# Kernel optimization log

Measured on AMD Instinct MI355X. Metric: run time of the kernel, lower is better.

The kernel has to match this reference:

```python
import jax, jax.numpy as jnp
import numpy as np

# dims
B, T, D, H, DFF, NTYPE = 8, 1024, 512, 8, 1024, 341
HD = D // H                    # 64 head dim
NUM_AXES = 1
DPR = D // H // (NUM_AXES + 1) # 32 dims rotated per axis
EPS = 1e-5
THETA = 10000.0


def layernorm(x, g, b):
    m = jnp.mean(x, axis=-1, keepdims=True)
    v = jnp.mean((x - m) ** 2, axis=-1, keepdims=True)
    return (x - m) * jax.lax.rsqrt(v + EPS) * g + b


def swiglu(x):
    a, gate = jnp.split(x, 2, axis=-1)
    return jax.nn.silu(gate) * a


def apply_rope(x, pos):
    # x: [B,H,T,DPR], pos: [B,T] float positions (possibly non-integer / scrambled order)
    inv_freq = 1.0 / (THETA ** (jnp.arange(0, DPR, 2, dtype=jnp.float32) / DPR))  # [DPR/2]
    freqs = pos[:, None, :, None] * inv_freq          # [B,1,T,DPR/2]
    cos = jnp.repeat(jnp.cos(freqs), 2, axis=-1)      # each freq repeated twice -> [B,1,T,DPR]
    sin = jnp.repeat(jnp.sin(freqs), 2, axis=-1)
    x1 = x[..., 0::2]
    x2 = x[..., 1::2]
    rot = jnp.stack([-x2, x1], axis=-1).reshape(x.shape)  # rotate_half, interleaved pairs
    return x * cos + rot * sin


def setup_inputs() -> dict:
    key = jax.random.key(0)
    ks = jax.random.split(key, 16)
    s = lambda d: 1.0 / np.sqrt(d)
    return {
        "x_type": jax.random.randint(ks[0], (B, T + 1), 0, NTYPE),
        "x_value": jax.random.normal(ks[1], (B, T, D), dtype=jnp.float32),
        "seq_order": jax.random.uniform(ks[2], (B, T + 1), dtype=jnp.float32) * T,
        "W_attn": jax.random.normal(ks[3], (D, 3 * D), dtype=jnp.float32) * s(D),
        "type_emb": jax.random.normal(ks[4], (NTYPE, 2 * D), dtype=jnp.float32) * 0.02,
        "ln1_g": jnp.ones((D,), jnp.float32),
        "ln1_b": jnp.zeros((D,), jnp.float32),
        "ln2_g": jnp.ones((D,), jnp.float32),
        "ln2_b": jnp.zeros((D,), jnp.float32),
        "W1": jax.random.normal(ks[5], (D, 2 * DFF), dtype=jnp.float32) * s(D),
        "b1": jnp.zeros((2 * DFF,), jnp.float32),
        "W2": jax.random.normal(ks[6], (DFF, D), dtype=jnp.float32) * s(DFF),
        "b2": jnp.zeros((D,), jnp.float32),
    }


def reference(x_type, x_value, seq_order, W_attn, type_emb, ln1_g, ln1_b, ln2_g, ln2_b, W1, b1, W2, b2):
    # --- attention sublayer ---
    h = layernorm(x_value, ln1_g, ln1_b)                  # [B,T,D]
    qkv = h @ W_attn                                      # [B,T,3D]
    q, k, v = jnp.split(qkv, 3, axis=-1)
    emb = type_emb[x_type]                                # [B,T+1,2D]
    q_embed, k_embed = jnp.split(emb, 2, axis=-1)
    q = q + q_embed[:, :-1]
    k = k + k_embed[:, 1:]
    # [B,H,T,HD]
    to_heads = lambda t: t.reshape(B, T, H, HD).transpose(0, 2, 1, 3)
    q, k, v = to_heads(q), to_heads(k), to_heads(v)
    # rotate first DPR dims with (shifted) seq_order; remaining dims untouched
    q = jnp.concatenate([apply_rope(q[..., :DPR], seq_order[:, :-1]), q[..., DPR:]], axis=-1)
    k = jnp.concatenate([apply_rope(k[..., :DPR], seq_order[:, 1:]), k[..., DPR:]], axis=-1)
    # causal SDPA
    scores = jnp.einsum("bhqd,bhkd->bhqk", q, k) / jnp.sqrt(jnp.float32(HD))
    causal = jnp.tril(jnp.ones((T, T), dtype=bool))
    scores = jnp.where(causal, scores, -jnp.inf)
    attn = jax.nn.softmax(scores, axis=-1)
    out = jnp.einsum("bhqk,bhkd->bhqd", attn, v)          # [B,H,T,HD]
    out = out.transpose(0, 2, 1, 3).reshape(B, T, D)
    x = x_value + out
    # --- SwiGLU FFN sublayer ---
    h2 = layernorm(x, ln2_g, ln2_b)
    ff = swiglu(h2 @ W1 + b1) @ W2 + b2
    return x + ff
```

## Files before the change

### kernel.cpp

```cpp
#include <hip/hip_runtime.h>
#include <stdint.h>
#include <math.h>

typedef unsigned short u16;
typedef unsigned int u32;
typedef __attribute__((ext_vector_type(8))) short bf16x8;
typedef __attribute__((ext_vector_type(4))) float f32x4;
typedef __attribute__((ext_vector_type(2))) float f32x2;
typedef __attribute__((ext_vector_type(2))) u16 u16x2;
typedef __attribute__((ext_vector_type(8))) u16 u16x8;
typedef __attribute__((ext_vector_type(2))) u32 u32x2;

#define B_ 8
#define T_ 1024
#define D_ 512
#define H_ 8
#define TP1 1025
#define QSCALE 0.1803368801111204f

__device__ __forceinline__ u16 f2b(float f) {
  union { float f; u32 u; } v; v.f = f;
  return (u16)((v.u + 0x7fffu + ((v.u >> 16) & 1u)) >> 16);
}
__device__ __forceinline__ void gld16(const void* g, void* l) {
  __builtin_amdgcn_global_load_lds((const __attribute__((address_space(1))) u32*)g,
                                   (__attribute__((address_space(3))) u32*)l, 16, 0, 0);
}
__device__ __forceinline__ f32x4 mfma16(bf16x8 a, bf16x8 b, f32x4 c) {
  return __builtin_amdgcn_mfma_f32_16x16x32_bf16(a, b, c, 0, 0, 0);
}
__device__ __forceinline__ u32 cvtpk(float lo, float hi) {
  u32 r;
  asm("v_cvt_pk_bf16_f32 %0, %1, %2" : "=v"(r) : "v"(lo), "v"(hi));
  return r;
}
union U8 { u32 u[4]; bf16x8 v; };

#define WAITV(N) asm volatile("s_waitcnt vmcnt(" #N ")" ::: "memory")

__global__ __launch_bounds__(256) void prep_kernel(const float* __restrict__ W_attn,
    const float* __restrict__ W1, const float* __restrict__ W2,
    const float* __restrict__ seq,
    u16* __restrict__ WtA, u16* __restrict__ W1i, u16* __restrict__ W2t,
    float* __restrict__ cq, float* __restrict__ sq_,
    float* __restrict__ ck, float* __restrict__ sk) {
  int bid = blockIdx.x, tid = threadIdx.x;
  if (bid >= 576) {
    int i = (bid - 576) * 256 + tid;
    int p = i & 15, bt = i >> 4, b = bt >> 10, t = bt & 1023;
    float inv = expf(-(float)p * 0.5756462732485115f);
    float aq = seq[b * TP1 + t] * inv;
    float ak = seq[b * TP1 + t + 1] * inv;
    cq[i] = cosf(aq); sq_[i] = sinf(aq);
    ck[i] = cosf(ak); sk[i] = sinf(ak);
    return;
  }
  __shared__ u16 lt[64][65];
  const float* src; u16* dst; int ld, Kd, k0, r0; bool ilv = false;
  if (bid < 192) {
    src = W_attn; dst = WtA; ld = 1536; Kd = 512;
    k0 = (bid & 7) * 64; r0 = (bid >> 3) * 64;
  } else if (bid < 448) {
    int t = bid - 192;
    src = W1; dst = W1i; ld = 2048; Kd = 512; ilv = true;
    k0 = (t & 7) * 64; r0 = (t >> 3) * 64;
  } else {
    int t = bid - 448;
    src = W2; dst = W2t; ld = 512; Kd = 1024;
    k0 = (t & 15) * 64; r0 = (t >> 4) * 64;
  }
  int nl = tid & 63;
  int scol, rloc;
  if (ilv) {
    if (nl < 32) { scol = (r0 >> 1) + nl;          rloc = ((nl >> 4) << 5) + (nl & 15); }
    else         { scol = 1024 + (r0 >> 1) + (nl - 32); rloc = (((nl - 32) >> 4) << 5) + 16 + (nl & 15); }
  } else { scol = r0 + nl; rloc = nl; }
  #pragma unroll
  for (int it = 0; it < 16; it++) {
    int kl = (tid >> 6) * 16 + it;
    lt[rloc][kl] = f2b(src[(size_t)(k0 + kl) * ld + scol]);
  }
  __syncthreads();
  #pragma unroll
  for (int it = 0; it < 16; it++) {
    int rl = (tid >> 6) * 16 + it;
    dst[(size_t)(r0 + rl) * Kd + k0 + nl] = lt[rl][nl];
  }
}

__global__ __launch_bounds__(256) void ln_kernel(const float* __restrict__ x,
    const float* __restrict__ g, const float* __restrict__ bta, u16* __restrict__ out) {
  int row = blockIdx.x * 4 + (threadIdx.x >> 6);
  int lane = threadIdx.x & 63;
  const float* xr = x + (size_t)row * D_ + lane * 8;
  f32x4 v0 = *(const f32x4*)xr;
  f32x4 v1 = *(const f32x4*)(xr + 4);
  float s = 0.f, sq = 0.f;
  #pragma unroll
  for (int j = 0; j < 4; j++) { s += v0[j] + v1[j]; sq += v0[j] * v0[j] + v1[j] * v1[j]; }
  #pragma unroll
  for (int m = 1; m < 64; m <<= 1) { s += __shfl_xor(s, m); sq += __shfl_xor(sq, m); }
  float mean = s * (1.f / D_);
  float var = sq * (1.f / D_) - mean * mean;
  float rstd = rsqrtf(var + 1e-5f);
  f32x4 g0 = *(const f32x4*)(g + lane * 8);
  f32x4 g1 = *(const f32x4*)(g + lane * 8 + 4);
  f32x4 b0 = *(const f32x4*)(bta + lane * 8);
  f32x4 b1 = *(const f32x4*)(bta + lane * 8 + 4);
  u16x8 o;
  #pragma unroll
  for (int j = 0; j < 4; j++) {
    o[j]     = f2b((v0[j] - mean) * rstd * g0[j] + b0[j]);
    o[4 + j] = f2b((v1[j] - mean) * rstd * g1[j] + b1[j]);
  }
  *(u16x8*)(out + (size_t)row * D_ + lane * 8) = o;
}


__global__ __launch_bounds__(256) void gemm_qkv(const u16* __restrict__ A,
    const u16* __restrict__ Bt,
    const int* __restrict__ x_type, const float* __restrict__ type_emb,
    const float* __restrict__ rqc, const float* __restrict__ rqs,
    const float* __restrict__ rkc, const float* __restrict__ rks,
    u16* __restrict__ qT, u16* __restrict__ kT, u16* __restrict__ vT) {
  __shared__ u16 lA[3][4096];
  __shared__ u16 lB[3][4096];
  const int K = 512, NK = 16;
  const int tid = threadIdx.x, lane = tid & 63, w = tid >> 6;
  const int wm = w >> 1, wn = w & 1;
  int swz = (blockIdx.x & 7) * 96 + (blockIdx.x >> 3);
  int byy = swz / 12, bxx = swz - byy * 12;
  const size_t bm = (size_t)byy * 128;
  const size_t bn = (size_t)bxx * 128;

  const int r0 = tid >> 2;
  const int cs = ((tid & 3) ^ ((r0 >> 1) & 3)) * 8;
  const u16* a0 = A + (bm + r0) * K + cs;
  const u16* a1 = A + (bm + 64 + r0) * K + cs;
  const u16* b0 = Bt + (bn + r0) * K + cs;
  const u16* b1p = Bt + (bn + 64 + r0) * K + cs;

  int aoff[4], boff[4];
  #pragma unroll
  for (int i = 0; i < 4; i++) {
    int ra = wm * 64 + i * 16 + (lane & 15);
    aoff[i] = ra * 64 + (((lane >> 4) ^ ((ra >> 1) & 3)) * 16);
    int rb = wn * 64 + i * 16 + (lane & 15);
    boff[i] = rb * 64 + (((lane >> 4) ^ ((rb >> 1) & 3)) * 16);
  }

  auto stage = [&](int j, int buf) {
    char* ad = (char*)lA + buf * 8192 + w * 1024;
    char* bd = (char*)lB + buf * 8192 + w * 1024;
    gld16(a0 + j * 32, ad);
    gld16(a1 + j * 32, ad + 4096);
    gld16(b0 + j * 32, bd);
    gld16(b1p + j * 32, bd + 4096);
  };
  f32x4 acc[4][4] = {};
  auto compute = [&](int buf) {
    const char* lAc = (const char*)lA + buf * 8192;
    const char* lBc = (const char*)lB + buf * 8192;
    bf16x8 af[4], bf[4];
    #pragma unroll
    for (int i = 0; i < 4; i++) af[i] = *(const bf16x8*)(lAc + aoff[i]);
    #pragma unroll
    for (int n = 0; n < 4; n++) bf[n] = *(const bf16x8*)(lBc + boff[n]);
    __builtin_amdgcn_s_setprio(1);
    #pragma unroll
    for (int i = 0; i < 4; i++)
      #pragma unroll
      for (int n = 0; n < 4; n++)
        acc[i][n] = mfma16(af[i], bf[n], acc[i][n]);
    __builtin_amdgcn_s_setprio(0);
  };

  stage(0, 0);
  stage(1, 1);
  int cur = 0;
  for (int j = 0; j < NK - 1; j++) {
    WAITV(4);
    __builtin_amdgcn_s_barrier();
    if (j + 2 < NK) { int nb = cur + 2; if (nb >= 3) nb -= 3; stage(j + 2, nb); }
    compute(cur);
    cur = (cur + 1 == 3) ? 0 : cur + 1;
  }
  WAITV(0);
  __builtin_amdgcn_s_barrier();
  compute(cur);

  const int region = (int)(bn >> 9);
  #pragma unroll
  for (int i = 0; i < 4; i++) {
    #pragma unroll
    for (int jj = 0; jj < 4; jj++) {
      int row = (int)bm + wm * 64 + i * 16 + (lane >> 4) * 4 + jj;
      int b = row >> 10, t = row & 1023;
      if (region == 0) {
        int ty = x_type[b * TP1 + t];
        #pragma unroll
        for (int n = 0; n < 4; n++) {
          int cloc = (int)bn + wn * 64 + n * 16 + (lane & 15);
          int h = cloc >> 6, hd = cloc & 63;
          float v = acc[i][n][jj] + type_emb[(size_t)ty * 1024 + cloc];
          float vp = __shfl_xor(v, 1);
          if (hd < 32) {
            int p = hd >> 1;
            float c = rqc[row * 16 + p], s = rqs[row * 16 + p];
            v = (hd & 1) ? (v * c + vp * s) : (v * c - vp * s);
          }
          qT[((size_t)(b * 8 + h) * T_ + t) * 64 + hd] = f2b(v * QSCALE);
        }
      } else if (region == 1) {
        int ty = x_type[b * TP1 + t + 1];
        #pragma unroll
        for (int n = 0; n < 4; n++) {
          int cloc = (int)bn - 512 + wn * 64 + n * 16 + (lane & 15);
          int h = cloc >> 6, hd = cloc & 63;
          float v = acc[i][n][jj] + type_emb[(size_t)ty * 1024 + 512 + cloc];
          float vp = __shfl_xor(v, 1);
          if (hd < 32) {
            int p = hd >> 1;
            float c = rkc[row * 16 + p], s = rks[row * 16 + p];
            v = (hd & 1) ? (v * c + vp * s) : (v * c - vp * s);
          }
          kT[((size_t)(b * 8 + h) * T_ + t) * 64 + hd] = f2b(v);
        }
      } else {
        #pragma unroll
        for (int n = 0; n < 4; n++) {
          int cloc = (int)bn - 1024 + wn * 64 + n * 16 + (lane & 15);
          int h = cloc >> 6, hd = cloc & 63;
          vT[((size_t)(b * 8 + h) * 64 + hd) * T_ + t] = f2b(acc[i][n][jj]);
        }
      }
    }
  }
}

__global__ __launch_bounds__(256) void gemm_ff1(const u16* __restrict__ A,
    const u16* __restrict__ Bt, const float* __restrict__ b1,
    u16* __restrict__ outp) {
  __shared__ u16 lA[3][4096];
  __shared__ u16 lB[3][4096];
  const int K = 512, NK = 16;
  const int tid = threadIdx.x, lane = tid & 63, w = tid >> 6;
  const int wm = w >> 1, wn = w & 1;
  int swz = (blockIdx.x & 7) * 128 + (blockIdx.x >> 3);
  int byy = swz >> 4, bxx = swz & 15;
  const size_t bm = (size_t)byy * 128;
  const size_t bn = (size_t)bxx * 128;

  const int r0 = tid >> 2;
  const int cs = ((tid & 3) ^ ((r0 >> 1) & 3)) * 8;
  const u16* a0 = A + (bm + r0) * K + cs;
  const u16* a1 = A + (bm + 64 + r0) * K + cs;
  const u16* b0 = Bt + (bn + r0) * K + cs;
  const u16* b1p = Bt + (bn + 64 + r0) * K + cs;

  int aoff[4], boff[4];
  #pragma unroll
  for (int i = 0; i < 4; i++) {
    int ra = wm * 64 + i * 16 + (lane & 15);
    aoff[i] = ra * 64 + (((lane >> 4) ^ ((ra >> 1) & 3)) * 16);
    int rb = wn * 64 + i * 16 + (lane & 15);
    boff[i] = rb * 64 + (((lane >> 4) ^ ((rb >> 1) & 3)) * 16);
  }

  auto stage = [&](int j, int buf) {
    char* ad = (char*)lA + buf * 8192 + w * 1024;
    char* bd = (char*)lB + buf * 8192 + w * 1024;
    gld16(a0 + j * 32, ad);
    gld16(a1 + j * 32, ad + 4096);
    gld16(b0 + j * 32, bd);
    gld16(b1p + j * 32, bd + 4096);
  };
  f32x4 acc[4][4] = {};
  auto compute = [&](int buf) {
    const char* lAc = (const char*)lA + buf * 8192;
    const char* lBc = (const char*)lB + buf * 8192;
    bf16x8 af[4], bf[4];
    #pragma unroll
    for (int i = 0; i < 4; i++) af[i] = *(const bf16x8*)(lAc + aoff[i]);
    #pragma unroll
    for (int n = 0; n < 4; n++) bf[n] = *(const bf16x8*)(lBc + boff[n]);
    __builtin_amdgcn_s_setprio(1);
    #pragma unroll
    for (int i = 0; i < 4; i++)
      #pragma unroll
      for (int n = 0; n < 4; n++)
        acc[i][n] = mfma16(af[i], bf[n], acc[i][n]);
    __builtin_amdgcn_s_setprio(0);
  };

  stage(0, 0);
  stage(1, 1);
  int cur = 0;
  for (int j = 0; j < NK - 1; j++) {
    WAITV(4);
    __builtin_amdgcn_s_barrier();
    if (j + 2 < NK) { int nb = cur + 2; if (nb >= 3) nb -= 3; stage(j + 2, nb); }
    compute(cur);
    cur = (cur + 1 == 3) ? 0 : cur + 1;
  }
  WAITV(0);
  __builtin_amdgcn_s_barrier();
  compute(cur);

  #pragma unroll
  for (int np = 0; np < 2; np++) {
    int c = ((int)bn >> 1) + wn * 32 + np * 16 + (lane & 15);
    float bav = b1[c], bgv = b1[1024 + c];
    #pragma unroll
    for (int i = 0; i < 4; i++) {
      #pragma unroll
      for (int jj = 0; jj < 4; jj++) {
        int row = (int)bm + wm * 64 + i * 16 + (lane >> 4) * 4 + jj;
        float av = acc[i][2 * np][jj] + bav;
        float gv = acc[i][2 * np + 1][jj] + bgv;
        float sg = gv / (1.f + expf(-gv));
        outp[(size_t)row * 1024 + c] = f2b(sg * av);
      }
    }
  }
}

__global__ __launch_bounds__(512) void gemm_ff2(const u16* __restrict__ A,
    const u16* __restrict__ Bt, const float* __restrict__ bias,
    float* __restrict__ C) {
  __shared__ u16 lA[3][4096];
  __shared__ u16 lB[3][4096];
  const int K = 1024, N = 512, NK = 32;
  const int tid = threadIdx.x, lane = tid & 63, w = tid >> 6;
  const int wm = w >> 2, wn = w & 3;
  int swz = (blockIdx.x & 7) * 32 + (blockIdx.x >> 3);
  int byy = swz >> 2, bxx = swz & 3;
  const size_t bm = (size_t)byy * 128;
  const size_t bn = (size_t)bxx * 128;

  const int r0 = tid >> 2;
  const int cs = ((tid & 3) ^ ((r0 >> 1) & 3)) * 8;
  const u16* a0 = A + (bm + r0) * K + cs;
  const u16* b0 = Bt + (bn + r0) * K + cs;

  int aoff[4], boff[2];
  #pragma unroll
  for (int i = 0; i < 4; i++) {
    int ra = wm * 64 + i * 16 + (lane & 15);
    aoff[i] = ra * 64 + (((lane >> 4) ^ ((ra >> 1) & 3)) * 16);
  }
  #pragma unroll
  for (int n = 0; n < 2; n++) {
    int rb = wn * 32 + n * 16 + (lane & 15);
    boff[n] = rb * 64 + (((lane >> 4) ^ ((rb >> 1) & 3)) * 16);
  }

  auto stage = [&](int j, int buf) {
    gld16(a0 + j * 32, (char*)lA + buf * 8192 + w * 1024);
    gld16(b0 + j * 32, (char*)lB + buf * 8192 + w * 1024);
  };
  f32x4 acc[4][2] = {};
  auto compute = [&](int buf) {
    const char* lAc = (const char*)lA + buf * 8192;
    const char* lBc = (const char*)lB + buf * 8192;
    bf16x8 af[4], bf[2];
    #pragma unroll
    for (int i = 0; i < 4; i++) af[i] = *(const bf16x8*)(lAc + aoff[i]);
    #pragma unroll
    for (int n = 0; n < 2; n++) bf[n] = *(const bf16x8*)(lBc + boff[n]);
    __builtin_amdgcn_s_setprio(1);
    #pragma unroll
    for (int i = 0; i < 4; i++)
      #pragma unroll
      for (int n = 0; n < 2; n++)
        acc[i][n] = mfma16(af[i], bf[n], acc[i][n]);
    __builtin_amdgcn_s_setprio(0);
  };

  stage(0, 0);
  stage(1, 1);
  int cur = 0;
  for (int j = 0; j < NK - 1; j++) {
    WAITV(2);
    __builtin_amdgcn_s_barrier();
    if (j + 2 < NK) { int nb = cur + 2; if (nb >= 3) nb -= 3; stage(j + 2, nb); }
    compute(cur);
    cur = (cur + 1 == 3) ? 0 : cur + 1;
  }
  WAITV(0);
  __builtin_amdgcn_s_barrier();
  compute(cur);

  #pragma unroll
  for (int i = 0; i < 4; i++) {
    size_t mrow = bm + wm * 64 + i * 16 + (lane >> 4) * 4;
    #pragma unroll
    for (int n = 0; n < 2; n++) {
      size_t col = bn + wn * 32 + n * 16 + (lane & 15);
      float bv = bias[col];
      #pragma unroll
      for (int jj = 0; jj < 4; jj++) {
        size_t idx = (mrow + jj) * (size_t)N + col;
        C[idx] = acc[i][n][jj] + bv + C[idx];
      }
    }
  }
}

__global__ __launch_bounds__(512) void attn_kernel(const u16* __restrict__ qT,
    const u16* __restrict__ kT, const u16* __restrict__ vT,
    const float* __restrict__ xv, float* __restrict__ X) {
  int s0 = (blockIdx.x & 7) * 64 + (blockIdx.x >> 3);
  const int bh = s0 >> 3;
  const int qp = 7 - (s0 & 7);
  const int b = bh >> 3, h = bh & 7;
  const int tid = threadIdx.x, lane = tid & 63, w = tid >> 6;
  const int q = lane & 15, g = lane >> 4;
  __shared__ u16 lK[3][4096];
  __shared__ u16 lV[3][4096];

  const int qrow0 = qp * 128 + w * 16;
  bf16x8 qf[2];
  {
    const u16* qp_ = qT + ((size_t)bh * T_ + qrow0 + q) * 64 + g * 8;
    qf[0] = *(const bf16x8*)qp_;
    qf[1] = *(const bf16x8*)(qp_ + 32);
  }
  f32x4 acc[4] = {};
  float mr = -1e30f, lr = 0.f;

  const int sr = tid >> 3;
  const int scs = ((tid & 7) ^ (sr & 7)) * 8;
  const u16* kb = kT + ((size_t)bh * T_ + sr) * 64 + scs;
  const u16* vb = vT + ((size_t)bh * 64 + sr) * T_ + scs;

  auto stage = [&](int j, int buf) {
    gld16(kb + (size_t)j * 4096, (char*)lK + buf * 8192 + w * 1024);
    gld16(vb + j * 64, (char*)lV + buf * 8192 + w * 1024);
  };
  auto compute = [&](int j, int buf) {
    const char* lKc = (const char*)lK + buf * 8192;
    const char* lVc = (const char*)lV + buf * 8192;
    if (j * 64 > qrow0 + 15) return;
    f32x4 s[4] = {};
    __builtin_amdgcn_s_setprio(1);
    #pragma unroll
    for (int ka = 0; ka < 2; ka++) {
      #pragma unroll
      for (int n = 0; n < 4; n++) {
        bf16x8 kf = *(const bf16x8*)(lKc + (n * 16 + q) * 128 +
                                     (((ka * 4 + g) ^ (q & 7)) * 16));
        s[n] = mfma16(kf, qf[ka], s[n]);
      }
    }
    __builtin_amdgcn_s_setprio(0);
    if (j * 64 + 63 > qrow0) {
      int qrow = qrow0 + q;
      #pragma unroll
      for (int n = 0; n < 4; n++)
        #pragma unroll
        for (int i = 0; i < 4; i++)
          if (j * 64 + n * 16 + g * 4 + i > qrow) s[n][i] = -1e30f;
    }
    float mt = fmaxf(fmaxf(fmaxf(s[0][0], s[0][1]), fmaxf(s[0][2], s[0][3])),
                     fmaxf(fmaxf(s[1][0], s[1][1]), fmaxf(s[1][2], s[1][3])));
    mt = fmaxf(mt, fmaxf(fmaxf(fmaxf(s[2][0], s[2][1]), fmaxf(s[2][2], s[2][3])),
                         fmaxf(fmaxf(s[3][0], s[3][1]), fmaxf(s[3][2], s[3][3]))));
    mt = fmaxf(mt, __shfl_xor(mt, 16));
    mt = fmaxf(mt, __shfl_xor(mt, 32));
    if (__any(mt > mr + 8.f)) {
      float mnew = fmaxf(mr, mt);
      float sc = exp2f(mr - mnew);
      mr = mnew;
      lr *= sc;
      #pragma unroll
      for (int t = 0; t < 4; t++) acc[t] *= sc;
    }
    float p[4][4];
    float ps = 0.f;
    #pragma unroll
    for (int n = 0; n < 4; n++)
      #pragma unroll
      for (int i = 0; i < 4; i++) { p[n][i] = exp2f(s[n][i] - mr); ps += p[n][i]; }
    ps += __shfl_xor(ps, 16);
    ps += __shfl_xor(ps, 32);
    lr += ps;
    U8 pa[2];
    #pragma unroll
    for (int kt = 0; kt < 2; kt++) {
      pa[kt].u[0] = cvtpk(p[2 * kt][0], p[2 * kt][1]);
      pa[kt].u[1] = cvtpk(p[2 * kt][2], p[2 * kt][3]);
      pa[kt].u[2] = cvtpk(p[2 * kt + 1][0], p[2 * kt + 1][1]);
      pa[kt].u[3] = cvtpk(p[2 * kt + 1][2], p[2 * kt + 1][3]);
    }
    __builtin_amdgcn_s_setprio(1);
    #pragma unroll
    for (int t = 0; t < 4; t++) {
      const char* vr = lVc + (t * 16 + q) * 128 + (g & 1) * 8;
      #pragma unroll
      for (int kt = 0; kt < 2; kt++) {
        u32x2 lo = *(const u32x2*)(vr + (((kt * 4 + (g >> 1)) ^ (q & 7)) * 16));
        u32x2 hi = *(const u32x2*)(vr + (((kt * 4 + 2 + (g >> 1)) ^ (q & 7)) * 16));
        U8 af;
        af.u[0] = lo[0]; af.u[1] = lo[1]; af.u[2] = hi[0]; af.u[3] = hi[1];
        acc[t] = mfma16(af.v, pa[kt].v, acc[t]);
      }
    }
    __builtin_amdgcn_s_setprio(0);
  };

  const int jmax = 2 * qp + 2;
  stage(0, 0);
  stage(1, 1);
  int cur = 0;
  for (int j = 0; j < jmax - 1; j++) {
    WAITV(2);
    __builtin_amdgcn_s_barrier();
    if (j + 2 < jmax) { int nb = cur + 2; if (nb >= 3) nb -= 3; stage(j + 2, nb); }
    compute(j, cur);
    cur = (cur + 1 == 3) ? 0 : cur + 1;
  }
  WAITV(0);
  __builtin_amdgcn_s_barrier();
  compute(jmax - 1, cur);

  {
    float inv = 1.f / lr;
    size_t base = ((size_t)b * T_ + qrow0 + q) * D_ + h * 64 + g * 4;
    #pragma unroll
    for (int t = 0; t < 4; t++) {
      f32x4 r = *(const f32x4*)(xv + base + t * 16);
      f32x4 o;
      #pragma unroll
      for (int i = 0; i < 4; i++) o[i] = r[i] + acc[t][i] * inv;
      *(f32x4*)(X + base + t * 16) = o;
    }
  }
}

extern "C" void kernel_launch(void* const* d_in, const int* in_sizes, int n_in,
                              void* d_out, int out_size, void* d_ws, size_t ws_size,
                              hipStream_t stream) {
  const int*   x_type   = (const int*)d_in[0];
  const float* x_value  = (const float*)d_in[1];
  const float* seq      = (const float*)d_in[2];
  const float* W_attn   = (const float*)d_in[3];
  const float* type_emb = (const float*)d_in[4];
  const float* ln1_g    = (const float*)d_in[5];
  const float* ln1_b    = (const float*)d_in[6];
  const float* ln2_g    = (const float*)d_in[7];
  const float* ln2_b    = (const float*)d_in[8];
  const float* W1       = (const float*)d_in[9];
  const float* b1       = (const float*)d_in[10];
  const float* W2       = (const float*)d_in[11];
  const float* b2       = (const float*)d_in[12];
  float* out = (float*)d_out;
  char* ws = (char*)d_ws;

  u16*   WtA  = (u16*)(ws + 0);
  u16*   W1i  = (u16*)(ws + 1572864);
  u16*   W2t  = (u16*)(ws + 3670016);
  float* rqc  = (float*)(ws + 4718592);
  float* rqs  = (float*)(ws + 5242880);
  float* rkc  = (float*)(ws + 5767168);
  float* rks  = (float*)(ws + 6291456);
  u16*   hbuf = (u16*)(ws + 6815744);
  u16*   qTb  = (u16*)(ws + 15204352);
  u16*   kTb  = (u16*)(ws + 23592960);
  u16*   vTb  = (u16*)(ws + 31981568);
  u16*   ff1a = (u16*)(ws + 15204352);

  prep_kernel<<<1088, 256, 0, stream>>>(W_attn, W1, W2, seq, WtA, W1i, W2t,
                                        rqc, rqs, rkc, rks);
  ln_kernel<<<B_ * T_ / 4, 256, 0, stream>>>(x_value, ln1_g, ln1_b, hbuf);
  gemm_qkv<<<768, 256, 0, stream>>>(hbuf, WtA, x_type, type_emb,
                                    rqc, rqs, rkc, rks, qTb, kTb, vTb);
  attn_kernel<<<512, 512, 0, stream>>>(qTb, kTb, vTb, x_value, out);
  ln_kernel<<<B_ * T_ / 4, 256, 0, stream>>>(out, ln2_g, ln2_b, hbuf);
  gemm_ff1<<<1024, 256, 0, stream>>>(hbuf, W1i, b1, ff1a);
  gemm_ff2<<<256, 512, 0, stream>>>(ff1a, W2t, b2, out);
}
```

Measured before the change: 143.3 us.

## Use 128-key tiles with double buffering and XCD-local head mapping in attention

The causal attention kernel now processes keys in 128-wide tiles instead of 64-wide ones. It swaps the three-stage buffered pipeline with explicit wait counts for a two-buffer scheme that calls __syncthreads once per tile. Block indices are remapped so each XCD handles a contiguous group of (batch, head) pairs, and the launch-bounds hint requests higher occupancy. The goal is fewer loop iterations and barriers, plus better K/V cache locality per XCD. In exchange, waves now compute the whole diagonal tile even where their rows are fully masked, and load latency is hidden less deeply.

```diff
diff --git a/kernel.cpp b/kernel.cpp
--- a/kernel.cpp
+++ b/kernel.cpp
@@ -115,7 +115,6 @@
   }
   *(u16x8*)(out + (size_t)row * D_ + lane * 8) = o;
 }
-
 
 __global__ __launch_bounds__(256) void gemm_qkv(const u16* __restrict__ A,
     const u16* __restrict__ Bt,
@@ -407,17 +406,19 @@
   }
 }
 
-__global__ __launch_bounds__(512) void attn_kernel(const u16* __restrict__ qT,
+__global__ __launch_bounds__(512, 4) void attn_kernel(const u16* __restrict__ qT,
     const u16* __restrict__ kT, const u16* __restrict__ vT,
     const float* __restrict__ xv, float* __restrict__ X) {
   int s0 = (blockIdx.x & 7) * 64 + (blockIdx.x >> 3);
-  const int bh = s0 >> 3;
-  const int qp = 7 - (s0 & 7);
+  const int xcd = blockIdx.x & 7;
+  (void)xcd;
+  const int bh = ((blockIdx.x & 7) << 3) + (s0 & 7);
+  const int qp = 7 - ((s0 >> 3) & 7);
   const int b = bh >> 3, h = bh & 7;
   const int tid = threadIdx.x, lane = tid & 63, w = tid >> 6;
   const int q = lane & 15, g = lane >> 4;
-  __shared__ u16 lK[3][4096];
-  __shared__ u16 lV[3][4096];
+  __shared__ u16 lK[2][8192];
+  __shared__ u16 lV[2][8192];
 
   const int qrow0 = qp * 128 + w * 16;
   bf16x8 qf[2];
@@ -435,37 +436,47 @@
   const u16* vb = vT + ((size_t)bh * 64 + sr) * T_ + scs;
 
   auto stage = [&](int j, int buf) {
-    gld16(kb + (size_t)j * 4096, (char*)lK + buf * 8192 + w * 1024);
-    gld16(vb + j * 64, (char*)lV + buf * 8192 + w * 1024);
-  };
-  auto compute = [&](int j, int buf) {
-    const char* lKc = (const char*)lK + buf * 8192;
-    const char* lVc = (const char*)lV + buf * 8192;
-    if (j * 64 > qrow0 + 15) return;
-    f32x4 s[4] = {};
+    char* kd = (char*)lK + buf * 16384 + w * 1024;
+    char* vd = (char*)lV + buf * 16384 + w * 1024;
+    gld16(kb + (size_t)j * 8192, kd);
+    gld16(kb + (size_t)j * 8192 + 4096, kd + 8192);
+    gld16(vb + j * 128, vd);
+    gld16(vb + j * 128 + 64, vd + 8192);
+  };
+
+  const int jmax = qp + 1;
+  stage(0, 0);
+  __syncthreads();
+  int cur = 0;
+  for (int j = 0; j < jmax; j++) {
+    if (j + 1 < jmax) stage(j + 1, cur ^ 1);
+    const char* lKc = (const char*)lK + cur * 16384;
+    const char* lVc = (const char*)lV + cur * 16384;
+
+    f32x4 s[8] = {};
     __builtin_amdgcn_s_setprio(1);
     #pragma unroll
     for (int ka = 0; ka < 2; ka++) {
       #pragma unroll
-      for (int n = 0; n < 4; n++) {
-        bf16x8 kf = *(const bf16x8*)(lKc + (n * 16 + q) * 128 +
+      for (int n = 0; n < 8; n++) {
+        bf16x8 kf = *(const bf16x8*)(lKc + (n >> 2) * 8192 + ((n & 3) * 16 + q) * 128 +
                                      (((ka * 4 + g) ^ (q & 7)) * 16));
         s[n] = mfma16(kf, qf[ka], s[n]);
       }
     }
     __builtin_amdgcn_s_setprio(0);
-    if (j * 64 + 63 > qrow0) {
-      int qrow = qrow0 + q;
-      #pragma unroll
-      for (int n = 0; n < 4; n++)
+    if (j == jmax - 1) {
+      int qrow = w * 16 + q;
+      #pragma unroll
+      for (int n = 0; n < 8; n++)
         #pragma unroll
         for (int i = 0; i < 4; i++)
-          if (j * 64 + n * 16 + g * 4 + i > qrow) s[n][i] = -1e30f;
-    }
-    float mt = fmaxf(fmaxf(fmaxf(s[0][0], s[0][1]), fmaxf(s[0][2], s[0][3])),
-                     fmaxf(fmaxf(s[1][0], s[1][1]), fmaxf(s[1][2], s[1][3])));
-    mt = fmaxf(mt, fmaxf(fmaxf(fmaxf(s[2][0], s[2][1]), fmaxf(s[2][2], s[2][3])),
-                         fmaxf(fmaxf(s[3][0], s[3][1]), fmaxf(s[3][2], s[3][3]))));
+          if (n * 16 + g * 4 + i > qrow) s[n][i] = -1e30f;
+    }
+    float mt = -1e30f;
+    #pragma unroll
+    for (int n = 0; n < 8; n++)
+      mt = fmaxf(mt, fmaxf(fmaxf(s[n][0], s[n][1]), fmaxf(s[n][2], s[n][3])));
     mt = fmaxf(mt, __shfl_xor(mt, 16));
     mt = fmaxf(mt, __shfl_xor(mt, 32));
     if (__any(mt > mr + 8.f)) {
@@ -476,54 +487,43 @@
       #pragma unroll
       for (int t = 0; t < 4; t++) acc[t] *= sc;
     }
-    float p[4][4];
     float ps = 0.f;
-    #pragma unroll
-    for (int n = 0; n < 4; n++)
-      #pragma unroll
-      for (int i = 0; i < 4; i++) { p[n][i] = exp2f(s[n][i] - mr); ps += p[n][i]; }
+    U8 pa[4];
+    #pragma unroll
+    for (int kt = 0; kt < 4; kt++) {
+      float p0[4], p1[4];
+      #pragma unroll
+      for (int i = 0; i < 4; i++) {
+        p0[i] = exp2f(s[2 * kt][i] - mr);
+        p1[i] = exp2f(s[2 * kt + 1][i] - mr);
+        ps += p0[i] + p1[i];
+      }
+      pa[kt].u[0] = cvtpk(p0[0], p0[1]);
+      pa[kt].u[1] = cvtpk(p0[2], p0[3]);
+      pa[kt].u[2] = cvtpk(p1[0], p1[1]);
+      pa[kt].u[3] = cvtpk(p1[2], p1[3]);
+    }
     ps += __shfl_xor(ps, 16);
     ps += __shfl_xor(ps, 32);
     lr += ps;
-    U8 pa[2];
-    #pragma unroll
-    for (int kt = 0; kt < 2; kt++) {
-      pa[kt].u[0] = cvtpk(p[2 * kt][0], p[2 * kt][1]);
-      pa[kt].u[1] = cvtpk(p[2 * kt][2], p[2 * kt][3]);
-      pa[kt].u[2] = cvtpk(p[2 * kt + 1][0], p[2 * kt + 1][1]);
-      pa[kt].u[3] = cvtpk(p[2 * kt + 1][2], p[2 * kt + 1][3]);
-    }
     __builtin_amdgcn_s_setprio(1);
     #pragma unroll
     for (int t = 0; t < 4; t++) {
-      const char* vr = lVc + (t * 16 + q) * 128 + (g & 1) * 8;
-      #pragma unroll
-      for (int kt = 0; kt < 2; kt++) {
-        u32x2 lo = *(const u32x2*)(vr + (((kt * 4 + (g >> 1)) ^ (q & 7)) * 16));
-        u32x2 hi = *(const u32x2*)(vr + (((kt * 4 + 2 + (g >> 1)) ^ (q & 7)) * 16));
+      #pragma unroll
+      for (int kt = 0; kt < 4; kt++) {
+        const char* vrh = lVc + (kt >> 1) * 8192 + (t * 16 + q) * 128 + (g & 1) * 8;
+        int ktl = kt & 1;
+        u32x2 lo = *(const u32x2*)(vrh + (((ktl * 4 + (g >> 1)) ^ (q & 7)) * 16));
+        u32x2 hi = *(const u32x2*)(vrh + (((ktl * 4 + 2 + (g >> 1)) ^ (q & 7)) * 16));
         U8 af;
         af.u[0] = lo[0]; af.u[1] = lo[1]; af.u[2] = hi[0]; af.u[3] = hi[1];
         acc[t] = mfma16(af.v, pa[kt].v, acc[t]);
       }
     }
     __builtin_amdgcn_s_setprio(0);
-  };
-
-  const int jmax = 2 * qp + 2;
-  stage(0, 0);
-  stage(1, 1);
-  int cur = 0;
-  for (int j = 0; j < jmax - 1; j++) {
-    WAITV(2);
-    __builtin_amdgcn_s_barrier();
-    if (j + 2 < jmax) { int nb = cur + 2; if (nb >= 3) nb -= 3; stage(j + 2, nb); }
-    compute(j, cur);
-    cur = (cur + 1 == 3) ? 0 : cur + 1;
-  }
-  WAITV(0);
-  __builtin_amdgcn_s_barrier();
-  compute(jmax - 1, cur);
-
+    __syncthreads();
+    cur ^= 1;
+  }
   {
     float inv = 1.f / lr;
     size_t base = ((size_t)b * T_ + qrow0 + q) * D_ + h * 64 + g * 4;
```

Result: faster. 134.0 us (-6.5%).
